# Optimization experiments

Hardware: AMD Instinct MI355X
Metric: run time of the kernel (lower is better)

Reference implementation:

```python
import jax, jax.numpy as jnp
import numpy as np

MATRIX_SIZE = 64  # m; chol params T = m*(m+1)//2 = 2080
INPUT_SIZE = 512
BATCH = 8192


def setup_inputs() -> dict:
    key = jax.random.key(0)
    k1, k2, k3 = jax.random.split(key, 3)
    T = MATRIX_SIZE * (MATRIX_SIZE + 1) // 2
    x = jax.random.normal(k1, (BATCH, INPUT_SIZE), dtype=jnp.float32)
    # nn.Linear params: W [T, input_size], b [T]
    W = jax.random.normal(k2, (T, INPUT_SIZE), dtype=jnp.float32) / np.sqrt(INPUT_SIZE)
    b = jax.random.normal(k3, (T,), dtype=jnp.float32) * 0.01
    return {"x": x, "W": W, "b": b}


def reference(x, W, b):
    m = MATRIX_SIZE
    # fc: [B, T] Cholesky parameters
    chol = x @ W.T + b
    # Row-major lower-triangle ordering (i, j<=i) matches the original idx loop
    rows, cols = np.tril_indices(m)           # each [T]
    diag = jnp.asarray(rows == cols)           # [T] bool
    # ReLU on diagonal entries, identity off-diagonal (single fused where)
    vals = jnp.where(diag[None, :], jax.nn.relu(chol), chol)  # [B, T]
    B = x.shape[0]
    L = jnp.zeros((B, m, m), dtype=chol.dtype).at[:, rows, cols].set(vals)
    # L @ L^T per batch element -> positive semidefinite [B, m, m]
    return jnp.einsum('bij,bkj->bik', L, L)
```

## Files before the change

kernel.cpp:

```cpp
#include <hip/hip_runtime.h>
#include <stdint.h>

#define MDIM 8192
#define KDIM 512
#define TDIM 2080
#define NPAD 2176
#define MSZ  64
#define NSC  1040

typedef __attribute__((ext_vector_type(8))) __bf16 bf16x8;
typedef __attribute__((ext_vector_type(4))) float  f32x4;

__device__ __forceinline__ unsigned short f2bf(float f) {
    unsigned int u = __float_as_uint(f);
    u += 0x7fffu + ((u >> 16) & 1u);
    return (unsigned short)(u >> 16);
}

__device__ __forceinline__ int tril_row(int n) {
    int i = (int)((sqrtf((float)(8 * n + 1)) - 1.0f) * 0.5f);
    while ((i + 1) * (i + 2) / 2 <= n) ++i;
    while (i * (i + 1) / 2 > n) --i;
    return i;
}

__device__ __forceinline__ int swz_addr(int i, int j) {
    int ch = ((j >> 3) ^ i) & 7;
    return i * 128 + (ch << 4) + ((j & 7) * 2);
}

#define NX4 (MDIM * KDIM / 4)
#define NW4 (NPAD * KDIM / 4)
#define NT4 (NPAD / 4)

__global__ __launch_bounds__(256) void convert_kernel(const float* __restrict__ x,
                                                      const float* __restrict__ W,
                                                      const float* __restrict__ b,
                                                      unsigned short* __restrict__ xb,
                                                      unsigned short* __restrict__ wb,
                                                      float* __restrict__ biasf,
                                                      float* __restrict__ diagm,
                                                      unsigned int* __restrict__ sidx) {
    int idx = blockIdx.x * 256 + threadIdx.x;
    if (idx < NX4) {
        float4 v = reinterpret_cast<const float4*>(x)[idx];
        reinterpret_cast<ushort4*>(xb)[idx] =
            make_ushort4(f2bf(v.x), f2bf(v.y), f2bf(v.z), f2bf(v.w));
    } else if (idx < NX4 + NW4) {
        int j = idx - NX4;
        int n = (j * 4) >> 9;
        ushort4 o = make_ushort4(0, 0, 0, 0);
        if (n < TDIM) {
            float4 v = reinterpret_cast<const float4*>(W)[j];
            o = make_ushort4(f2bf(v.x), f2bf(v.y), f2bf(v.z), f2bf(v.w));
        }
        reinterpret_cast<ushort4*>(wb)[j] = o;
    } else if (idx < NX4 + NW4 + NT4) {
        int t = idx - NX4 - NW4;
#pragma unroll
        for (int r = 0; r < 4; ++r) {
            int n = t * 4 + r;
            float bv = 0.f, dm = 0.f;
            if (n < TDIM) {
                bv = b[n];
                int i = tril_row(n);
                dm = (n - i * (i + 1) / 2 == i) ? 1.f : 0.f;
            }
            biasf[n] = bv;
            diagm[n] = dm;
        }
    } else {
        int t = idx - NX4 - NW4 - NT4;
        if (t < NSC) {
            int n = 2 * t;
            int i = tril_row(n);
            int j = n - i * (i + 1) / 2;
            int a0 = swz_addr(i, j);
            int i2 = i, j2 = j + 1;
            if (j2 > i2) { i2 = i + 1; j2 = 0; }
            int a1 = swz_addr(i2, j2);
            sidx[t] = (unsigned int)a0 | ((unsigned int)a1 << 16);
        }
    }
}

typedef __attribute__((address_space(1))) void as1_void;
typedef __attribute__((address_space(3))) void as3_void;

__device__ __forceinline__ void gload_lds16(const void* g, void* l) {
    __builtin_amdgcn_global_load_lds((as1_void*)(void*)g, (as3_void*)l, 16, 0, 0);
}

__device__ __forceinline__ bf16x8 frag_load(const unsigned short* base, int row, int kbyte) {
    kbyte ^= (row & 7) << 4;
    return *reinterpret_cast<const bf16x8*>(reinterpret_cast<const char*>(base) + row * 128 + kbyte);
}

__global__ __launch_bounds__(256, 4) void gemm_kernel(const unsigned short* __restrict__ xb,
                                                      const unsigned short* __restrict__ wb,
                                                      const float* __restrict__ biasf,
                                                      const float* __restrict__ diagm,
                                                      unsigned short* __restrict__ chol) {
    __shared__ __align__(16) unsigned short As[128 * 64];
    __shared__ __align__(16) unsigned short Bs[128 * 64];
    const int tid  = threadIdx.x;
    const int lane = tid & 63;
    const int wave = tid >> 6;

    const int bid = blockIdx.x;
    const int xcd = bid & 7;
    const int c   = bid >> 3;
    const int mt  = xcd * 8 + c / 17;
    const int nt  = c % 17;
    const int m0 = mt * 128;
    const int n0 = nt * 128;

    const int wm = (wave >> 1) * 64;
    const int wn = (wave & 1) * 64;
    const int lr = lane & 15;
    const int lq = lane >> 4;

    f32x4 acc[4][4];
    f32x4 zero = {0.f, 0.f, 0.f, 0.f};
#pragma unroll
    for (int i = 0; i < 4; ++i)
#pragma unroll
        for (int j = 0; j < 4; ++j) acc[i][j] = zero;

    for (int k0 = 0; k0 < KDIM; k0 += 64) {
        const unsigned short* ga = xb + (size_t)m0 * KDIM + k0;
        const unsigned short* gb = wb + (size_t)n0 * KDIM + k0;
#pragma unroll
        for (int cc = 0; cc < 4; ++cc) {
            int flat = cc * 256 + tid;
            int row  = flat >> 3;
            int ch   = (flat & 7) ^ (row & 7);
            unsigned short* lb = (unsigned short*)As + (size_t)(cc * 256 + (tid & 192)) * 8;
            gload_lds16(ga + row * KDIM + ch * 8, lb);
        }
#pragma unroll
        for (int cc = 0; cc < 4; ++cc) {
            int flat = cc * 256 + tid;
            int row  = flat >> 3;
            int ch   = (flat & 7) ^ (row & 7);
            unsigned short* lb = (unsigned short*)Bs + (size_t)(cc * 256 + (tid & 192)) * 8;
            gload_lds16(gb + row * KDIM + ch * 8, lb);
        }
        __syncthreads();
#pragma unroll
        for (int kk = 0; kk < 2; ++kk) {
            bf16x8 af[4], bf[4];
            int kb = kk * 64 + lq * 16;
#pragma unroll
            for (int i = 0; i < 4; ++i) {
                af[i] = frag_load(As, wm + i * 16 + lr, kb);
                bf[i] = frag_load(Bs, wn + i * 16 + lr, kb);
            }
#pragma unroll
            for (int mi = 0; mi < 4; ++mi)
#pragma unroll
                for (int ni = 0; ni < 4; ++ni)
                    acc[mi][ni] = __builtin_amdgcn_mfma_f32_16x16x32_bf16(bf[ni], af[mi], acc[mi][ni], 0, 0, 0);
        }
        __syncthreads();
    }

    const float4* bt = reinterpret_cast<const float4*>(biasf);
    const float4* dt = reinterpret_cast<const float4*>(diagm);
#pragma unroll
    for (int ni = 0; ni < 4; ++ni) {
        int nb = n0 + wn + ni * 16 + lq * 4;
        float4 bv = bt[nb >> 2];
        float4 dm = dt[nb >> 2];
#pragma unroll
        for (int mi = 0; mi < 4; ++mi) {
            int m = m0 + wm + mi * 16 + lr;
            float v0 = acc[mi][ni][0] + bv.x; if (dm.x != 0.f && v0 < 0.f) v0 = 0.f;
            float v1 = acc[mi][ni][1] + bv.y; if (dm.y != 0.f && v1 < 0.f) v1 = 0.f;
            float v2 = acc[mi][ni][2] + bv.z; if (dm.z != 0.f && v2 < 0.f) v2 = 0.f;
            float v3 = acc[mi][ni][3] + bv.w; if (dm.w != 0.f && v3 < 0.f) v3 = 0.f;
            *reinterpret_cast<ushort4*>(&chol[(size_t)m * NPAD + nb]) =
                make_ushort4(f2bf(v0), f2bf(v1), f2bf(v2), f2bf(v3));
        }
    }
}

__global__ __launch_bounds__(256) void syrk_kernel(const unsigned short* __restrict__ chol,
                                                   const unsigned int* __restrict__ sidx,
                                                   float* __restrict__ out) {
    __shared__ __align__(16) unsigned short Ls[4][64 * 64];
    const int tid  = threadIdx.x;
    const int lane = tid & 63;
    const int wave = tid >> 6;

    const int bid = blockIdx.x;
    const int bb  = (bid & 7) * 256 + (bid >> 3);
    const int batch = bb * 4 + wave;
    unsigned short* L = Ls[wave];

    const unsigned int* row = reinterpret_cast<const unsigned int*>(chol + (size_t)batch * NPAD);
    unsigned int vals[17], adr[17];
#pragma unroll
    for (int c = 0; c < 17; ++c) {
        int t = lane + c * 64;
        vals[c] = (t < NSC) ? row[t] : 0u;
        adr[c]  = (t < NSC) ? sidx[t] : 0u;
    }

#pragma unroll
    for (int c = 0; c < 8; ++c)
        *reinterpret_cast<int4*>(reinterpret_cast<char*>(L) + (c * 64 + lane) * 16) = make_int4(0, 0, 0, 0);
    __builtin_amdgcn_sched_barrier(0);

#pragma unroll
    for (int c = 0; c < 17; ++c) {
        int t = lane + c * 64;
        if (t < NSC) {
            unsigned int v = vals[c];
            unsigned int a = adr[c];
            *reinterpret_cast<unsigned short*>(reinterpret_cast<char*>(L) + (a & 0xffffu)) =
                (unsigned short)(v & 0xffffu);
            *reinterpret_cast<unsigned short*>(reinterpret_cast<char*>(L) + (a >> 16)) =
                (unsigned short)(v >> 16);
        }
    }
    asm volatile("s_waitcnt lgkmcnt(0)" ::: "memory");
    __builtin_amdgcn_sched_barrier(0);

    const int lr = lane & 15;
    const int lq = lane >> 4;
    bf16x8 fr[4][2];
#pragma unroll
    for (int i = 0; i < 4; ++i)
#pragma unroll
        for (int kk = 0; kk < 2; ++kk)
            fr[i][kk] = frag_load(L, i * 16 + lr, kk * 64 + lq * 16);

    f32x4 acc[4][4];
    f32x4 zero = {0.f, 0.f, 0.f, 0.f};
#pragma unroll
    for (int i = 0; i < 4; ++i)
#pragma unroll
        for (int j = 0; j < 4; ++j) acc[i][j] = zero;

#pragma unroll
    for (int mi = 0; mi < 4; ++mi)
#pragma unroll
        for (int ni = 0; ni < 4; ++ni)
#pragma unroll
            for (int kk = 0; kk < 2; ++kk)
                acc[mi][ni] = __builtin_amdgcn_mfma_f32_16x16x32_bf16(fr[mi][kk], fr[ni][kk], acc[mi][ni], 0, 0, 0);

    float* fs = reinterpret_cast<float*>(L);
    float* ob = out + (size_t)batch * (MSZ * MSZ);
#pragma unroll
    for (int half = 0; half < 2; ++half) {
        asm volatile("s_waitcnt lgkmcnt(0)" ::: "memory");
        __builtin_amdgcn_sched_barrier(0);
#pragma unroll
        for (int ni2 = 0; ni2 < 2; ++ni2) {
            int ni = half * 2 + ni2;
            int r32 = ni2 * 16 + lr;
#pragma unroll
            for (int mi = 0; mi < 4; ++mi) {
                int byte = r32 * 256 + (mi * 16 + lq * 4) * 4;
                byte ^= (r32 & 7) << 4;
                *reinterpret_cast<f32x4*>(reinterpret_cast<char*>(fs) + byte) = acc[mi][ni];
            }
        }
        asm volatile("s_waitcnt lgkmcnt(0)" ::: "memory");
        __builtin_amdgcn_sched_barrier(0);
#pragma unroll
        for (int c = 0; c < 8; ++c) {
            int off  = c * 1024 + lane * 16;
            int r32  = off >> 8;
            int byte = off ^ ((r32 & 7) << 4);
            f32x4 v = *reinterpret_cast<const f32x4*>(reinterpret_cast<const char*>(fs) + byte);
            *reinterpret_cast<f32x4*>(reinterpret_cast<char*>(ob) + half * 8192 + off) = v;
        }
    }
}

extern "C" void kernel_launch(void* const* d_in, const int* in_sizes, int n_in,
                              void* d_out, int out_size, void* d_ws, size_t ws_size,
                              hipStream_t stream) {
    (void)in_sizes; (void)n_in; (void)out_size; (void)ws_size;
    const float* x = (const float*)d_in[0];
    const float* W = (const float*)d_in[1];
    const float* b = (const float*)d_in[2];
    float* out = (float*)d_out;

    unsigned short* xb   = (unsigned short*)d_ws;
    unsigned short* wb   = xb + (size_t)MDIM * KDIM;
    unsigned short* chol = wb + (size_t)NPAD * KDIM;
    float* biasf = (float*)(chol + (size_t)MDIM * NPAD);
    float* diagm = biasf + NPAD;
    unsigned int* sidx = (unsigned int*)(diagm + NPAD);

    int conv_blocks = (NX4 + NW4 + NT4 + NSC + 255) / 256;
    convert_kernel<<<dim3(conv_blocks), dim3(256), 0, stream>>>(x, W, b, xb, wb, biasf, diagm, sidx);
    gemm_kernel<<<dim3(17 * 64), dim3(256), 0, stream>>>(xb, wb, biasf, diagm, chol);
    syrk_kernel<<<dim3(MDIM / 4), dim3(256), 0, stream>>>(chol, sidx, out);
}
```

Measured before the change: 71.10 us.

## Fuse x fp32-to-bf16 conversion into GEMM A-tile loads

Drops the separate pass that converted x to bf16. The GEMM now streams fp32 x tiles straight into LDS with a swizzled layout and converts to bf16 with v_cvt_pk_bf16_f32 when loading fragments. This removes one read and one write of the x array, but doubles the A-tile LDS footprint and its global read bytes, and lowers the launch-bounds occupancy target from 4 to 3.

```diff
diff --git a/kernel.cpp b/kernel.cpp
--- a/kernel.cpp
+++ b/kernel.cpp
@@ -29,34 +29,26 @@
     return i * 128 + (ch << 4) + ((j & 7) * 2);
 }
 
-#define NX4 (MDIM * KDIM / 4)
 #define NW4 (NPAD * KDIM / 4)
 #define NT4 (NPAD / 4)
 
-__global__ __launch_bounds__(256) void convert_kernel(const float* __restrict__ x,
-                                                      const float* __restrict__ W,
-                                                      const float* __restrict__ b,
-                                                      unsigned short* __restrict__ xb,
-                                                      unsigned short* __restrict__ wb,
-                                                      float* __restrict__ biasf,
-                                                      float* __restrict__ diagm,
-                                                      unsigned int* __restrict__ sidx) {
+__global__ __launch_bounds__(256) void convertw_kernel(const float* __restrict__ W,
+                                                       const float* __restrict__ b,
+                                                       unsigned short* __restrict__ wb,
+                                                       float* __restrict__ biasf,
+                                                       float* __restrict__ diagm,
+                                                       unsigned int* __restrict__ sidx) {
     int idx = blockIdx.x * 256 + threadIdx.x;
-    if (idx < NX4) {
-        float4 v = reinterpret_cast<const float4*>(x)[idx];
-        reinterpret_cast<ushort4*>(xb)[idx] =
-            make_ushort4(f2bf(v.x), f2bf(v.y), f2bf(v.z), f2bf(v.w));
-    } else if (idx < NX4 + NW4) {
-        int j = idx - NX4;
-        int n = (j * 4) >> 9;
+    if (idx < NW4) {
+        int n = (idx * 4) >> 9;
         ushort4 o = make_ushort4(0, 0, 0, 0);
         if (n < TDIM) {
-            float4 v = reinterpret_cast<const float4*>(W)[j];
+            float4 v = reinterpret_cast<const float4*>(W)[idx];
             o = make_ushort4(f2bf(v.x), f2bf(v.y), f2bf(v.z), f2bf(v.w));
         }
-        reinterpret_cast<ushort4*>(wb)[j] = o;
-    } else if (idx < NX4 + NW4 + NT4) {
-        int t = idx - NX4 - NW4;
+        reinterpret_cast<ushort4*>(wb)[idx] = o;
+    } else if (idx < NW4 + NT4) {
+        int t = idx - NW4;
 #pragma unroll
         for (int r = 0; r < 4; ++r) {
             int n = t * 4 + r;
@@ -70,7 +62,7 @@
             diagm[n] = dm;
         }
     } else {
-        int t = idx - NX4 - NW4 - NT4;
+        int t = idx - NW4 - NT4;
         if (t < NSC) {
             int n = 2 * t;
             int i = tril_row(n);
@@ -96,12 +88,25 @@
     return *reinterpret_cast<const bf16x8*>(reinterpret_cast<const char*>(base) + row * 128 + kbyte);
 }
 
-__global__ __launch_bounds__(256, 4) void gemm_kernel(const unsigned short* __restrict__ xb,
+__device__ __forceinline__ bf16x8 frag_load_a(const float* base, int row, int kbyte) {
+    int byte = row * 256 + (kbyte ^ ((row & 7) << 5));
+    const char* p = reinterpret_cast<const char*>(base) + byte;
+    f32x4 lo = *reinterpret_cast<const f32x4*>(p);
+    f32x4 hi = *reinterpret_cast<const f32x4*>(p + 16);
+    union { unsigned int u[4]; bf16x8 v; } r;
+    asm("v_cvt_pk_bf16_f32 %0, %1, %2" : "=v"(r.u[0]) : "v"(lo[0]), "v"(lo[1]));
+    asm("v_cvt_pk_bf16_f32 %0, %1, %2" : "=v"(r.u[1]) : "v"(lo[2]), "v"(lo[3]));
+    asm("v_cvt_pk_bf16_f32 %0, %1, %2" : "=v"(r.u[2]) : "v"(hi[0]), "v"(hi[1]));
+    asm("v_cvt_pk_bf16_f32 %0, %1, %2" : "=v"(r.u[3]) : "v"(hi[2]), "v"(hi[3]));
+    return r.v;
+}
+
+__global__ __launch_bounds__(256, 3) void gemm_kernel(const float* __restrict__ x,
                                                       const unsigned short* __restrict__ wb,
                                                       const float* __restrict__ biasf,
                                                       const float* __restrict__ diagm,
                                                       unsigned short* __restrict__ chol) {
-    __shared__ __align__(16) unsigned short As[128 * 64];
+    __shared__ __align__(16) float          As[128 * 64];
     __shared__ __align__(16) unsigned short Bs[128 * 64];
     const int tid  = threadIdx.x;
     const int lane = tid & 63;
@@ -128,15 +133,15 @@
         for (int j = 0; j < 4; ++j) acc[i][j] = zero;
 
     for (int k0 = 0; k0 < KDIM; k0 += 64) {
-        const unsigned short* ga = xb + (size_t)m0 * KDIM + k0;
+        const float*          ga = x  + (size_t)m0 * KDIM + k0;
         const unsigned short* gb = wb + (size_t)n0 * KDIM + k0;
 #pragma unroll
-        for (int cc = 0; cc < 4; ++cc) {
+        for (int cc = 0; cc < 8; ++cc) {
             int flat = cc * 256 + tid;
-            int row  = flat >> 3;
-            int ch   = (flat & 7) ^ (row & 7);
-            unsigned short* lb = (unsigned short*)As + (size_t)(cc * 256 + (tid & 192)) * 8;
-            gload_lds16(ga + row * KDIM + ch * 8, lb);
+            int row  = flat >> 4;
+            int cs   = (flat & 15) ^ ((row & 7) << 1);
+            float* lb = As + (size_t)(cc * 256 + (tid & 192)) * 4;
+            gload_lds16(ga + (size_t)row * KDIM + cs * 4, lb);
         }
 #pragma unroll
         for (int cc = 0; cc < 4; ++cc) {
@@ -150,11 +155,10 @@
 #pragma unroll
         for (int kk = 0; kk < 2; ++kk) {
             bf16x8 af[4], bf[4];
-            int kb = kk * 64 + lq * 16;
 #pragma unroll
             for (int i = 0; i < 4; ++i) {
-                af[i] = frag_load(As, wm + i * 16 + lr, kb);
-                bf[i] = frag_load(Bs, wn + i * 16 + lr, kb);
+                af[i] = frag_load_a(As, wm + i * 16 + lr, kk * 128 + lq * 32);
+                bf[i] = frag_load(Bs, wn + i * 16 + lr, kk * 64 + lq * 16);
             }
 #pragma unroll
             for (int mi = 0; mi < 4; ++mi)
@@ -290,15 +294,14 @@
     const float* b = (const float*)d_in[2];
     float* out = (float*)d_out;
 
-    unsigned short* xb   = (unsigned short*)d_ws;
-    unsigned short* wb   = xb + (size_t)MDIM * KDIM;
+    unsigned short* wb   = (unsigned short*)d_ws;
     unsigned short* chol = wb + (size_t)NPAD * KDIM;
     float* biasf = (float*)(chol + (size_t)MDIM * NPAD);
     float* diagm = biasf + NPAD;
     unsigned int* sidx = (unsigned int*)(diagm + NPAD);
 
-    int conv_blocks = (NX4 + NW4 + NT4 + NSC + 255) / 256;
-    convert_kernel<<<dim3(conv_blocks), dim3(256), 0, stream>>>(x, W, b, xb, wb, biasf, diagm, sidx);
-    gemm_kernel<<<dim3(17 * 64), dim3(256), 0, stream>>>(xb, wb, biasf, diagm, chol);
+    int convw_blocks = (NW4 + NT4 + NSC + 255) / 256;
+    convertw_kernel<<<dim3(convw_blocks), dim3(256), 0, stream>>>(W, b, wb, biasf, diagm, sidx);
+    gemm_kernel<<<dim3(17 * 64), dim3(256), 0, stream>>>(x, wb, biasf, diagm, chol);
     syrk_kernel<<<dim3(MDIM / 4), dim3(256), 0, stream>>>(chol, sidx, out);
 }
```

Measured after the change: 74.76 us. 5.1% more time.
